# Kernel optimization log

Hardware: AMD Instinct MI355X
Metric: run time of the kernel (lower is better)

## Reference

```python
import jax, jax.numpy as jnp
import numpy as np
import math

NUM_HEADS = 8
EMBED = 512
D_K = EMBED // NUM_HEADS
B, T1, T2 = 16, 512, 512
N_POS = 2 * T1 - 1


def rel_shift(x, left_context=0):
    # x: (B, H, T1, 2*T1-1) -> (B, H, T1, T2), out[i, j] = x[i, j - i + T1 - 1]
    t1 = x.shape[2]
    t2 = t1 + left_context
    idx = jnp.arange(t2)[None, :] - jnp.arange(t1)[:, None] + (t1 - 1)  # (T1, T2)
    return jnp.take_along_axis(x, idx[None, None, :, :], axis=-1)


def setup_inputs() -> dict:
    key = jax.random.key(0)
    ks = jax.random.split(key, 16)
    scale = 1.0 / math.sqrt(EMBED)
    inp = {
        "query": jax.random.normal(ks[0], (B, T1, EMBED), jnp.float32),
        "key": jax.random.normal(ks[1], (B, T2, EMBED), jnp.float32),
        "value": jax.random.normal(ks[2], (B, T2, EMBED), jnp.float32),
        "pos_enc": jax.random.normal(ks[3], (B, N_POS, EMBED), jnp.float32),
        "mask": jnp.zeros((B, T2), dtype=bool),
        "chunk_mask": jnp.zeros((T1, T1), dtype=bool),
        "Wq": jax.random.normal(ks[4], (EMBED, EMBED), jnp.float32) * scale,
        "bq": jnp.zeros((EMBED,), jnp.float32),
        "Wk": jax.random.normal(ks[5], (EMBED, EMBED), jnp.float32) * scale,
        "bk": jnp.zeros((EMBED,), jnp.float32),
        "Wv": jax.random.normal(ks[6], (EMBED, EMBED), jnp.float32) * scale,
        "bv": jnp.zeros((EMBED,), jnp.float32),
        "Wpos": jax.random.normal(ks[7], (EMBED, EMBED), jnp.float32) * scale,
        "Wo": jax.random.normal(ks[8], (EMBED, EMBED), jnp.float32) * scale,
        "bo": jnp.zeros((EMBED,), jnp.float32),
        "pos_bias_u": jax.random.normal(ks[9], (NUM_HEADS, D_K), jnp.float32) * 0.1,
        "pos_bias_v": jax.random.normal(ks[10], (NUM_HEADS, D_K), jnp.float32) * 0.1,
        "left_context": 0,
    }
    return inp


def reference(query, key, value, pos_enc, mask, chunk_mask, Wq, bq, Wk, bk, Wv, bv,
              Wpos, Wo, bo, pos_bias_u, pos_bias_v, left_context):
    b, t1, _ = query.shape
    t2 = key.shape[1]
    # qkv projections -> (B, T, H, d_k)
    q = (query @ Wq.T + bq).reshape(b, t1, NUM_HEADS, D_K)
    k = (key @ Wk.T + bk).reshape(b, t2, NUM_HEADS, D_K)
    v = (value @ Wv.T + bv).reshape(b, t2, NUM_HEADS, D_K)
    # positional projection (no bias) -> (B, N, H, d_k)
    p = (pos_enc @ Wpos.T).reshape(b, -1, NUM_HEADS, D_K)
    # content and positional scores
    matrix_ac = jnp.einsum('bihd,bjhd->bhij', q + pos_bias_u, k)  # (B,H,T1,T2)
    matrix_bd = jnp.einsum('bihd,bnhd->bhin', q + pos_bias_v, p)  # (B,H,T1,N)
    matrix_bd = rel_shift(matrix_bd, left_context=left_context)   # (B,H,T1,T2)
    scores = (matrix_ac + matrix_bd) / math.sqrt(D_K)
    # combined mask: True = masked
    m = chunk_mask[None, None, :, :] | mask[:, None, None, :]
    neg_inf = jnp.finfo(scores.dtype).min
    scores = jnp.where(m, neg_inf, scores)
    attn = jax.nn.softmax(scores, axis=-1)
    attn = jnp.where(m, 0.0, attn)
    out = jnp.einsum('bhij,bjhd->bihd', attn, v).reshape(b, t1, NUM_HEADS * D_K)
    return out @ Wo.T + bo
```

## Files before the change

### kernel.cpp

```cpp
#include <hip/hip_runtime.h>
#include <math.h>

typedef _Float16 f16;
typedef f16 f16x8 __attribute__((ext_vector_type(8)));
typedef f16 f16x4 __attribute__((ext_vector_type(4)));
typedef float f32x4 __attribute__((ext_vector_type(4)));

#define H_   8
#define E_   512
#define DK   64
#define NPOS 1023

__device__ __forceinline__ f16x8 cvt8(const float4 a, const float4 b) {
    f16x8 h;
    h[0] = (f16)a.x; h[1] = (f16)a.y; h[2] = (f16)a.z; h[3] = (f16)a.w;
    h[4] = (f16)b.x; h[5] = (f16)b.y; h[6] = (f16)b.z; h[7] = (f16)b.w;
    return h;
}

struct PArg {
    const void* A; const float* W; const float* bias; const float* bias2;
    void* C; int Mvalid; int mode; int a16;
};
struct PArgs { PArg g[4]; };

__device__ __forceinline__ void gemm128_body(const PArg g, int bx, int by) {
    __shared__ __align__(16) f16 Al[2][128 * 32];
    __shared__ __align__(16) f16 Wl[2][128 * 32];
    const int tid = threadIdx.x;
    const int lane = tid & 63, w = tid >> 6;
    const int quad = lane >> 4, l15 = lane & 15;
    const int wr = w >> 1, wc = w & 1;
    const int m0 = by * 128, n0 = bx * 128;
    const int srow = tid >> 1, half = tid & 1;
    int arow = m0 + srow; if (arow >= g.Mvalid) arow = g.Mvalid - 1;
    const size_t aoff = (size_t)arow * 512 + half * 16;
    const size_t woff = (size_t)(n0 + srow) * 512 + half * 16;
    const int swr = (srow ^ (srow >> 2)) & 3;
    const int wo0 = srow * 32 + (((half * 2)     ^ swr) * 8);
    const int wo1 = srow * 32 + (((half * 2 + 1) ^ swr) * 8);
    const int swl = (l15 ^ (l15 >> 2)) & 3;
    const int rch = (quad ^ swl) * 8;

    f32x4 acc[4][4];
    #pragma unroll
    for (int m = 0; m < 4; ++m)
        #pragma unroll
        for (int n = 0; n < 4; ++n) acc[m][n] = (f32x4){0.f, 0.f, 0.f, 0.f};

    float4 fa0, fa1, fa2, fa3, fw0, fw1, fw2, fw3;
    uint4 ha0, ha1;

    #define LOADA(K0) do { \
        if (g.a16) { const f16* Ah = (const f16*)g.A + aoff + (K0); \
                     ha0 = *(const uint4*)Ah; ha1 = *(const uint4*)(Ah + 8); } \
        else { const float* Af = (const float*)g.A + aoff + (K0); \
               fa0 = *(const float4*)Af;       fa1 = *(const float4*)(Af + 4); \
               fa2 = *(const float4*)(Af + 8); fa3 = *(const float4*)(Af + 12); } } while (0)
    #define LOADW(K0) do { const float* Wf = g.W + woff + (K0); \
        fw0 = *(const float4*)Wf;        fw1 = *(const float4*)(Wf + 4); \
        fw2 = *(const float4*)(Wf + 8);  fw3 = *(const float4*)(Wf + 12); } while (0)
    #define STAGE(buf) do { \
        if (g.a16) { *(uint4*)&Al[buf][wo0] = ha0; *(uint4*)&Al[buf][wo1] = ha1; } \
        else { *(f16x8*)&Al[buf][wo0] = cvt8(fa0, fa1); *(f16x8*)&Al[buf][wo1] = cvt8(fa2, fa3); } \
        *(f16x8*)&Wl[buf][wo0] = cvt8(fw0, fw1); *(f16x8*)&Wl[buf][wo1] = cvt8(fw2, fw3); } while (0)

    LOADA(0); LOADW(0);
    STAGE(0);
    LOADA(32); LOADW(32);
    __syncthreads();

    #pragma unroll 2
    for (int ki = 0; ki < 16; ++ki) {
        const int cur = ki & 1, nxt = cur ^ 1;
        if (ki < 15) STAGE(nxt);
        if (ki < 14) { LOADA((ki + 2) * 32); LOADW((ki + 2) * 32); }
        f16x8 af[4], bf[4];
        #pragma unroll
        for (int m = 0; m < 4; ++m)
            af[m] = *(const f16x8*)&Al[cur][(wr * 64 + m * 16 + l15) * 32 + rch];
        #pragma unroll
        for (int n = 0; n < 4; ++n)
            bf[n] = *(const f16x8*)&Wl[cur][(wc * 64 + n * 16 + l15) * 32 + rch];
        #pragma unroll
        for (int m = 0; m < 4; ++m)
            #pragma unroll
            for (int n = 0; n < 4; ++n)
                acc[m][n] = __builtin_amdgcn_mfma_f32_16x16x32_f16(af[m], bf[n], acc[m][n], 0, 0, 0);
        __syncthreads();
    }
    #undef LOADA
    #undef LOADW
    #undef STAGE

    const int mq = m0 + wr * 64 + quad * 4;
    const int nq = n0 + wc * 64 + l15;
    #pragma unroll
    for (int m = 0; m < 4; ++m) {
        #pragma unroll
        for (int n = 0; n < 4; ++n) {
            const int gr0 = mq + m * 16;
            const int col = nq + n * 16;
            float bs = g.bias ? g.bias[col] : 0.f;
            if (g.bias2) bs += g.bias2[col];
            const f32x4 a = acc[m][n];
            if (g.mode == 0) {
                float* C = (float*)g.C;
                #pragma unroll
                for (int r = 0; r < 4; ++r) C[(size_t)(gr0 + r) * 512 + col] = a[r] + bs;
            } else if (g.mode == 1) {
                f16* C = (f16*)g.C;
                const int b = gr0 >> 9, t = gr0 & 511;
                const int hh = col >> 6, dk = col & 63;
                f16x4 hv;
                #pragma unroll
                for (int r = 0; r < 4; ++r) hv[r] = (f16)(a[r] + bs);
                *(f16x4*)&C[(((size_t)b * H_ + hh) * DK + dk) * 512 + t] = hv;
            } else if (g.mode == 2) {
                f16* C = (f16*)g.C;
                const int b = gr0 >> 9, t = gr0 & 511;
                const int hh = col >> 6, dk = col & 63;
                #pragma unroll
                for (int r = 0; r < 4; ++r)
                    C[(((size_t)b * H_ + hh) * 512 + t + r) * DK + dk] = (f16)(a[r] + bs);
            } else {
                f16* C = (f16*)g.C;
                const int hh = col >> 6, dk = col & 63;
                #pragma unroll
                for (int r = 0; r < 4; ++r) {
                    const int gm = gr0 + r;
                    if (gm < g.Mvalid) {
                        const int b = gm / NPOS, t = gm - b * NPOS;
                        C[(((size_t)b * H_ + hh) * NPOS + t) * DK + dk] = (f16)a[r];
                    }
                }
            }
        }
    }
}

__global__ __launch_bounds__(256, 3) void proj_all(PArgs a) {
    const int id = blockIdx.x;
    int gi, rem, nwg;
    if (id < 768) { gi = id >> 8; rem = id & 255; nwg = 256; }
    else          { gi = 3;       rem = id - 768; nwg = 512; }
    const int t = (rem & 7) * (nwg >> 3) + (rem >> 3);
    gemm128_body(a.g[gi], t & 3, t >> 2);
}
__global__ __launch_bounds__(256, 3) void proj_one(PArg g) {
    const int t = (blockIdx.x & 7) * 32 + (blockIdx.x >> 3);
    gemm128_body(g, t & 3, t >> 2);
}

__global__ __launch_bounds__(256) void attn_mfma(
    const f16* __restrict__ Qh,
    const f16* __restrict__ Kh,
    const f16* __restrict__ Vt,
    const f16* __restrict__ Ph,
    const float* __restrict__ pbu, const float* __restrict__ pbv,
    const unsigned char* __restrict__ bmask,
    const unsigned char* __restrict__ cmask,
    f16* __restrict__ CTX)
{
    __shared__ f16 Qa[64 * 72];
    __shared__ f16 Ka[64 * 72];
    __shared__ f16 Va[64 * 72];
    __shared__ f16 Pa[128 * 72];
    __shared__ unsigned char Ma[64 * 64];

    const int tid = threadIdx.x;
    const int lane = tid & 63, w = tid >> 6;
    const int quad = lane >> 4, l15 = lane & 15;
    const int id = blockIdx.x;
    const int lg = (id & 7) * 128 + (id >> 3);
    const int it = lg & 7, bh = lg >> 3;
    const int h = bh & 7, b = bh >> 3;
    const int i0 = it * 64;
    const int rowt = w * 16 + quad * 4;
    const int sr = tid >> 3, sc = (tid & 7) * 8;
    const int mr = tid >> 2, mc = (tid & 3) * 16;

    *(uint4*)&Qa[sr * 72 + sc] = *(const uint4*)&Qh[((size_t)bh * 512 + i0 + sr) * 64 + sc];
    *(uint4*)&Qa[(sr + 32) * 72 + sc] =
        *(const uint4*)&Qh[((size_t)bh * 512 + i0 + sr + 32) * 64 + sc];
    f16x8 dpbf[2];
    #pragma unroll
    for (int ks = 0; ks < 2; ++ks)
        #pragma unroll
        for (int j = 0; j < 8; ++j) {
            const int d = ks * 32 + quad * 8 + j;
            dpbf[ks][j] = (f16)(pbv[h * 64 + d] - pbu[h * 64 + d]);
        }

    float m_run[4], l_run[4];
    f32x4 accO[4];
    #pragma unroll
    for (int x = 0; x < 4; ++x) {
        m_run[x] = -__builtin_inff(); l_run[x] = 0.f;
        accO[x] = (f32x4){0.f, 0.f, 0.f, 0.f};
    }

    uint4 pK0, pK1, pV0, pV1, pP0, pP1, pP2, pP3, pM;
    {
        const int j0 = 0, nbase = 448 - i0;
        pK0 = *(const uint4*)&Kh[((size_t)bh * 512 + j0 + sr) * 64 + sc];
        pK1 = *(const uint4*)&Kh[((size_t)bh * 512 + j0 + sr + 32) * 64 + sc];
        pV0 = *(const uint4*)&Vt[((size_t)bh * 64 + sr) * 512 + j0 + sc];
        pV1 = *(const uint4*)&Vt[((size_t)bh * 64 + sr + 32) * 512 + j0 + sc];
        int n0_ = nbase + sr;       if (n0_ > NPOS - 1) n0_ = NPOS - 1;
        int n1_ = nbase + sr + 32;  if (n1_ > NPOS - 1) n1_ = NPOS - 1;
        int n2_ = nbase + sr + 64;  if (n2_ > NPOS - 1) n2_ = NPOS - 1;
        int n3_ = nbase + sr + 96;  if (n3_ > NPOS - 1) n3_ = NPOS - 1;
        pP0 = *(const uint4*)&Ph[((size_t)bh * NPOS + n0_) * 64 + sc];
        pP1 = *(const uint4*)&Ph[((size_t)bh * NPOS + n1_) * 64 + sc];
        pP2 = *(const uint4*)&Ph[((size_t)bh * NPOS + n2_) * 64 + sc];
        pP3 = *(const uint4*)&Ph[((size_t)bh * NPOS + n3_) * 64 + sc];
        const uint4 cm = *(const uint4*)&cmask[(size_t)(i0 + mr) * 512 + j0 + mc];
        const uint4 bm = *(const uint4*)&bmask[(size_t)b * 512 + j0 + mc];
        pM.x = cm.x | bm.x; pM.y = cm.y | bm.y; pM.z = cm.z | bm.z; pM.w = cm.w | bm.w;
    }

    for (int jt = 0; jt < 8; ++jt) {
        __syncthreads();
        *(uint4*)&Ka[sr * 72 + sc] = pK0;
        *(uint4*)&Ka[(sr + 32) * 72 + sc] = pK1;
        *(uint4*)&Va[sr * 72 + sc] = pV0;
        *(uint4*)&Va[(sr + 32) * 72 + sc] = pV1;
        *(uint4*)&Pa[sr * 72 + sc] = pP0;
        *(uint4*)&Pa[(sr + 32) * 72 + sc] = pP1;
        *(uint4*)&Pa[(sr + 64) * 72 + sc] = pP2;
        *(uint4*)&Pa[(sr + 96) * 72 + sc] = pP3;
        *(uint4*)&Ma[mr * 64 + mc] = pM;
        __syncthreads();

        if (jt < 7) {
            const int j0n = (jt + 1) * 64;
            const int nbase = j0n - i0 + 448;
            pK0 = *(const uint4*)&Kh[((size_t)bh * 512 + j0n + sr) * 64 + sc];
            pK1 = *(const uint4*)&Kh[((size_t)bh * 512 + j0n + sr + 32) * 64 + sc];
            pV0 = *(const uint4*)&Vt[((size_t)bh * 64 + sr) * 512 + j0n + sc];
            pV1 = *(const uint4*)&Vt[((size_t)bh * 64 + sr + 32) * 512 + j0n + sc];
            int n0_ = nbase + sr;       if (n0_ > NPOS - 1) n0_ = NPOS - 1;
            int n1_ = nbase + sr + 32;  if (n1_ > NPOS - 1) n1_ = NPOS - 1;
            int n2_ = nbase + sr + 64;  if (n2_ > NPOS - 1) n2_ = NPOS - 1;
            int n3_ = nbase + sr + 96;  if (n3_ > NPOS - 1) n3_ = NPOS - 1;
            pP0 = *(const uint4*)&Ph[((size_t)bh * NPOS + n0_) * 64 + sc];
            pP1 = *(const uint4*)&Ph[((size_t)bh * NPOS + n1_) * 64 + sc];
            pP2 = *(const uint4*)&Ph[((size_t)bh * NPOS + n2_) * 64 + sc];
            pP3 = *(const uint4*)&Ph[((size_t)bh * NPOS + n3_) * 64 + sc];
            const uint4 cm = *(const uint4*)&cmask[(size_t)(i0 + mr) * 512 + j0n + mc];
            const uint4 bm = *(const uint4*)&bmask[(size_t)b * 512 + j0n + mc];
            pM.x = cm.x | bm.x; pM.y = cm.y | bm.y; pM.z = cm.z | bm.z; pM.w = cm.w | bm.w;
        }

        f16x8 afQ[2], afV[2];
        #pragma unroll
        for (int ks = 0; ks < 2; ++ks) {
            afQ[ks] = *(const f16x8*)&Qa[(w * 16 + l15) * 72 + ks * 32 + quad * 8];
            afV[ks] = afQ[ks] + dpbf[ks];
        }
        f32x4 accAC[4];
        #pragma unroll
        for (int nt = 0; nt < 4; ++nt) {
            accAC[nt] = (f32x4){0.f, 0.f, 0.f, 0.f};
            #pragma unroll
            for (int ks = 0; ks < 2; ++ks) {
                const f16x8 bf = *(const f16x8*)&Ka[(nt * 16 + l15) * 72 + ks * 32 + quad * 8];
                accAC[nt] = __builtin_amdgcn_mfma_f32_16x16x32_f16(afQ[ks], bf, accAC[nt], 0, 0, 0);
            }
        }
        f32x4 accBD[5];
        #pragma unroll
        for (int u = 0; u < 5; ++u) {
            accBD[u] = (f32x4){0.f, 0.f, 0.f, 0.f};
            const int nts = (3 - w) + u;
            #pragma unroll
            for (int ks = 0; ks < 2; ++ks) {
                const f16x8 bf = *(const f16x8*)&Pa[(nts * 16 + l15) * 72 + ks * 32 + quad * 8];
                accBD[u] = __builtin_amdgcn_mfma_f32_16x16x32_f16(afV[ks], bf, accBD[u], 0, 0, 0);
            }
        }
        __syncthreads();

        #pragma unroll
        for (int rg = 0; rg < 4; ++rg) {
            const int qr = quad * 4 + rg;
            const int rt = rowt + rg;
            float tmpv[5];
            #pragma unroll
            for (int u = 0; u < 5; ++u) {
                const int cl = l15 + (3 + u) * 16 + qr - 63;
                const int dst = (quad * 16 + (cl & 15)) << 2;
                tmpv[u] = __uint_as_float(
                    (unsigned)__builtin_amdgcn_ds_permute(dst, (int)__float_as_uint(accBD[u][rg])));
            }
            const bool hi = l15 > qr;
            float sv[4]; unsigned mk = 0;
            #pragma unroll
            for (int nt = 0; nt < 4; ++nt) {
                const int c = nt * 16 + l15;
                const float bdv = hi ? tmpv[nt + 1] : tmpv[nt];
                float s = (accAC[nt][rg] + bdv) * 0.125f;
                if (Ma[rt * 64 + c]) { s = -3.402823466e38f; mk |= 1u << nt; }
                sv[nt] = s;
            }
            float tmax = fmaxf(fmaxf(sv[0], sv[1]), fmaxf(sv[2], sv[3]));
            #pragma unroll
            for (int d = 1; d < 16; d <<= 1) tmax = fmaxf(tmax, __shfl_xor(tmax, d));
            const float mnew = fmaxf(m_run[rg], tmax);
            const float alpha = __expf(m_run[rg] - mnew);
            float rsum = 0.f;
            f16 wv[4];
            #pragma unroll
            for (int nt = 0; nt < 4; ++nt) {
                const float e = __expf(sv[nt] - mnew);
                rsum += e;
                wv[nt] = ((mk >> nt) & 1u) ? (f16)0.f : (f16)e;
            }
            #pragma unroll
            for (int d = 1; d < 16; d <<= 1) rsum += __shfl_xor(rsum, d);
            l_run[rg] = l_run[rg] * alpha + rsum;
            m_run[rg] = mnew;
            #pragma unroll
            for (int dt = 0; dt < 4; ++dt) accO[dt][rg] *= alpha;
            #pragma unroll
            for (int nt = 0; nt < 4; ++nt)
                Ka[rt * 72 + nt * 16 + l15] = wv[nt];
        }
        f16x8 afW[2];
        #pragma unroll
        for (int ks = 0; ks < 2; ++ks)
            afW[ks] = *(const f16x8*)&Ka[(w * 16 + l15) * 72 + ks * 32 + quad * 8];
        #pragma unroll
        for (int dt = 0; dt < 4; ++dt)
            #pragma unroll
            for (int ks = 0; ks < 2; ++ks) {
                const f16x8 bf = *(const f16x8*)&Va[(dt * 16 + l15) * 72 + ks * 32 + quad * 8];
                accO[dt] = __builtin_amdgcn_mfma_f32_16x16x32_f16(afW[ks], bf, accO[dt], 0, 0, 0);
            }
    }

    #pragma unroll
    for (int rg = 0; rg < 4; ++rg) {
        const float inv = 1.0f / l_run[rg];
        const int gi = i0 + rowt + rg;
        #pragma unroll
        for (int dt = 0; dt < 4; ++dt)
            CTX[((size_t)b * 512 + gi) * 512 + h * 64 + dt * 16 + l15] = (f16)(accO[dt][rg] * inv);
    }
}

extern "C" void kernel_launch(void* const* d_in, const int* in_sizes, int n_in,
                              void* d_out, int out_size, void* d_ws, size_t ws_size,
                              hipStream_t stream) {
    const float* query   = (const float*)d_in[0];
    const float* key     = (const float*)d_in[1];
    const float* value   = (const float*)d_in[2];
    const float* pos_enc = (const float*)d_in[3];
    const unsigned char* mask       = (const unsigned char*)d_in[4];
    const unsigned char* chunk_mask = (const unsigned char*)d_in[5];
    const float* Wq  = (const float*)d_in[6];
    const float* bq  = (const float*)d_in[7];
    const float* Wk  = (const float*)d_in[8];
    const float* bk  = (const float*)d_in[9];
    const float* Wv  = (const float*)d_in[10];
    const float* bv  = (const float*)d_in[11];
    const float* Wpos = (const float*)d_in[12];
    const float* Wo   = (const float*)d_in[13];
    const float* bo   = (const float*)d_in[14];
    const float* pbu  = (const float*)d_in[15];
    const float* pbv  = (const float*)d_in[16];
    float* out = (float*)d_out;

    f16* base = (f16*)d_ws;
    size_t off = 0;
    f16* ctx = base + off; off += 4194304;
    f16* Qhm = base + off; off += 4194304;
    f16* Khm = base + off; off += 4194304;
    f16* Vtm = base + off; off += 4194304;
    f16* Phm = base + off; off += 8380416;

    PArgs pa;
    pa.g[0] = PArg{query,   Wq,   bq, pbu,     (void*)Qhm, 8192,  2, 0};
    pa.g[1] = PArg{key,     Wk,   bk, nullptr, (void*)Khm, 8192,  2, 0};
    pa.g[2] = PArg{value,   Wv,   bv, nullptr, (void*)Vtm, 8192,  1, 0};
    pa.g[3] = PArg{pos_enc, Wpos, nullptr, nullptr, (void*)Phm, 16368, 3, 0};
    proj_all<<<dim3(1280), 256, 0, stream>>>(pa);

    attn_mfma<<<dim3(1024), 256, 0, stream>>>(Qhm, Khm, Vtm, Phm, pbu, pbv,
                                              mask, chunk_mask, ctx);

    PArg go = PArg{ctx, Wo, bo, nullptr, (void*)out, 8192, 0, 1};
    proj_one<<<dim3(256), 256, 0, stream>>>(go);
}
```

Measured before the change: 287.6 us.

## Pre-convert inputs to fp16 and load GEMM tiles via global_load_lds

Adds a separate conversion kernel that casts all fp32 activations and weights to fp16 in workspace. The projection GEMMs then stream fp16 tiles directly into LDS with global_load_lds instead of loading fp32 into registers, converting and storing. This drops the double-buffered LDS, the swizzled layout and the register prefetch, and raises occupancy to 4 blocks. The trade-off is an extra full read and write pass over the inputs, plus a GEMM loop that no longer overlaps loads with MFMA and may now hit LDS bank conflicts.

```diff
diff --git a/kernel.cpp b/kernel.cpp
--- a/kernel.cpp
+++ b/kernel.cpp
@@ -11,36 +11,54 @@
 #define DK   64
 #define NPOS 1023
 
-__device__ __forceinline__ f16x8 cvt8(const float4 a, const float4 b) {
-    f16x8 h;
-    h[0] = (f16)a.x; h[1] = (f16)a.y; h[2] = (f16)a.z; h[3] = (f16)a.w;
-    h[4] = (f16)b.x; h[5] = (f16)b.y; h[6] = (f16)b.z; h[7] = (f16)b.w;
-    return h;
+#define GLL(SRC, DST) __builtin_amdgcn_global_load_lds( \
+    (const __attribute__((address_space(1))) void*)(SRC), \
+    (__attribute__((address_space(3))) void*)(DST), 16, 0, 0)
+
+struct CSeg { const float* src; f16* dst; int n4; };
+struct CArgs { CSeg s[9]; };
+__global__ __launch_bounds__(256) void conv_f16(CArgs a) {
+    const int stride = gridDim.x * 256;
+    const int gid = blockIdx.x * 256 + threadIdx.x;
+    for (int si = 0; si < 9; ++si) {
+        const float* __restrict__ src = a.s[si].src;
+        f16* __restrict__ dst = a.s[si].dst;
+        const int n4 = a.s[si].n4;
+        for (int i = gid; i < n4; i += stride) {
+            const float4 v = ((const float4*)src)[i];
+            f16x4 h; h[0] = (f16)v.x; h[1] = (f16)v.y; h[2] = (f16)v.z; h[3] = (f16)v.w;
+            ((f16x4*)dst)[i] = h;
+        }
+    }
 }
 
 struct PArg {
-    const void* A; const float* W; const float* bias; const float* bias2;
-    void* C; int Mvalid; int mode; int a16;
+    const f16* A; const f16* W; const float* bias; const float* bias2;
+    void* C; int Mvalid; int mode;
 };
 struct PArgs { PArg g[4]; };
 
 __device__ __forceinline__ void gemm128_body(const PArg g, int bx, int by) {
-    __shared__ __align__(16) f16 Al[2][128 * 32];
-    __shared__ __align__(16) f16 Wl[2][128 * 32];
+    __shared__ __align__(16) f16 Al[128 * 32];
+    __shared__ __align__(16) f16 Wl[128 * 32];
     const int tid = threadIdx.x;
     const int lane = tid & 63, w = tid >> 6;
     const int quad = lane >> 4, l15 = lane & 15;
     const int wr = w >> 1, wc = w & 1;
     const int m0 = by * 128, n0 = bx * 128;
-    const int srow = tid >> 1, half = tid & 1;
-    int arow = m0 + srow; if (arow >= g.Mvalid) arow = g.Mvalid - 1;
-    const size_t aoff = (size_t)arow * 512 + half * 16;
-    const size_t woff = (size_t)(n0 + srow) * 512 + half * 16;
-    const int swr = (srow ^ (srow >> 2)) & 3;
-    const int wo0 = srow * 32 + (((half * 2)     ^ swr) * 8);
-    const int wo1 = srow * 32 + (((half * 2 + 1) ^ swr) * 8);
-    const int swl = (l15 ^ (l15 >> 2)) & 3;
-    const int rch = (quad ^ swl) * 8;
+
+    const int r0 = w * 32 + (lane >> 2);
+    const int c0 = (lane & 3) * 8;
+    int ar0 = m0 + r0;      if (ar0 >= g.Mvalid) ar0 = g.Mvalid - 1;
+    int ar1 = m0 + r0 + 16; if (ar1 >= g.Mvalid) ar1 = g.Mvalid - 1;
+    const f16* A0 = g.A + (size_t)ar0 * 512 + c0;
+    const f16* A1 = g.A + (size_t)ar1 * 512 + c0;
+    const f16* W0 = g.W + (size_t)(n0 + r0) * 512 + c0;
+    const f16* W1 = g.W + (size_t)(n0 + r0 + 16) * 512 + c0;
+    f16* const lA0 = &Al[(w * 32) * 32];
+    f16* const lA1 = &Al[(w * 32 + 16) * 32];
+    f16* const lW0 = &Wl[(w * 32) * 32];
+    f16* const lW1 = &Wl[(w * 32 + 16) * 32];
 
     f32x4 acc[4][4];
     #pragma unroll
@@ -48,50 +66,28 @@
         #pragma unroll
         for (int n = 0; n < 4; ++n) acc[m][n] = (f32x4){0.f, 0.f, 0.f, 0.f};
 
-    float4 fa0, fa1, fa2, fa3, fw0, fw1, fw2, fw3;
-    uint4 ha0, ha1;
-
-    #define LOADA(K0) do { \
-        if (g.a16) { const f16* Ah = (const f16*)g.A + aoff + (K0); \
-                     ha0 = *(const uint4*)Ah; ha1 = *(const uint4*)(Ah + 8); } \
-        else { const float* Af = (const float*)g.A + aoff + (K0); \
-               fa0 = *(const float4*)Af;       fa1 = *(const float4*)(Af + 4); \
-               fa2 = *(const float4*)(Af + 8); fa3 = *(const float4*)(Af + 12); } } while (0)
-    #define LOADW(K0) do { const float* Wf = g.W + woff + (K0); \
-        fw0 = *(const float4*)Wf;        fw1 = *(const float4*)(Wf + 4); \
-        fw2 = *(const float4*)(Wf + 8);  fw3 = *(const float4*)(Wf + 12); } while (0)
-    #define STAGE(buf) do { \
-        if (g.a16) { *(uint4*)&Al[buf][wo0] = ha0; *(uint4*)&Al[buf][wo1] = ha1; } \
-        else { *(f16x8*)&Al[buf][wo0] = cvt8(fa0, fa1); *(f16x8*)&Al[buf][wo1] = cvt8(fa2, fa3); } \
-        *(f16x8*)&Wl[buf][wo0] = cvt8(fw0, fw1); *(f16x8*)&Wl[buf][wo1] = cvt8(fw2, fw3); } while (0)
-
-    LOADA(0); LOADW(0);
-    STAGE(0);
-    LOADA(32); LOADW(32);
-    __syncthreads();
-
-    #pragma unroll 2
     for (int ki = 0; ki < 16; ++ki) {
-        const int cur = ki & 1, nxt = cur ^ 1;
-        if (ki < 15) STAGE(nxt);
-        if (ki < 14) { LOADA((ki + 2) * 32); LOADW((ki + 2) * 32); }
+        const int k0 = ki * 32;
+        if (ki) __syncthreads();
+        GLL(A0 + k0, lA0);
+        GLL(A1 + k0, lA1);
+        GLL(W0 + k0, lW0);
+        GLL(W1 + k0, lW1);
+        __syncthreads();
+
         f16x8 af[4], bf[4];
         #pragma unroll
         for (int m = 0; m < 4; ++m)
-            af[m] = *(const f16x8*)&Al[cur][(wr * 64 + m * 16 + l15) * 32 + rch];
+            af[m] = *(const f16x8*)&Al[(wr * 64 + m * 16 + l15) * 32 + quad * 8];
         #pragma unroll
         for (int n = 0; n < 4; ++n)
-            bf[n] = *(const f16x8*)&Wl[cur][(wc * 64 + n * 16 + l15) * 32 + rch];
+            bf[n] = *(const f16x8*)&Wl[(wc * 64 + n * 16 + l15) * 32 + quad * 8];
         #pragma unroll
         for (int m = 0; m < 4; ++m)
             #pragma unroll
             for (int n = 0; n < 4; ++n)
                 acc[m][n] = __builtin_amdgcn_mfma_f32_16x16x32_f16(af[m], bf[n], acc[m][n], 0, 0, 0);
-        __syncthreads();
-    }
-    #undef LOADA
-    #undef LOADW
-    #undef STAGE
+    }
 
     const int mq = m0 + wr * 64 + quad * 4;
     const int nq = n0 + wc * 64 + l15;
@@ -139,7 +135,7 @@
     }
 }
 
-__global__ __launch_bounds__(256, 3) void proj_all(PArgs a) {
+__global__ __launch_bounds__(256, 4) void proj_all(PArgs a) {
     const int id = blockIdx.x;
     int gi, rem, nwg;
     if (id < 768) { gi = id >> 8; rem = id & 255; nwg = 256; }
@@ -147,7 +143,7 @@
     const int t = (rem & 7) * (nwg >> 3) + (rem >> 3);
     gemm128_body(a.g[gi], t & 3, t >> 2);
 }
-__global__ __launch_bounds__(256, 3) void proj_one(PArg g) {
+__global__ __launch_bounds__(256, 4) void proj_one(PArg g) {
     const int t = (blockIdx.x & 7) * 32 + (blockIdx.x >> 3);
     gemm128_body(g, t & 3, t >> 2);
 }
@@ -374,22 +370,43 @@
 
     f16* base = (f16*)d_ws;
     size_t off = 0;
-    f16* ctx = base + off; off += 4194304;
-    f16* Qhm = base + off; off += 4194304;
-    f16* Khm = base + off; off += 4194304;
-    f16* Vtm = base + off; off += 4194304;
-    f16* Phm = base + off; off += 8380416;
+    f16* ctx  = base + off; off += 4194304;
+    f16* Qhm  = base + off; off += 4194304;
+    f16* Khm  = base + off; off += 4194304;
+    f16* Vtm  = base + off; off += 4194304;
+    f16* Phm  = base + off; off += 8380416;
+    f16* qf   = base + off; off += 4194304;
+    f16* kf   = base + off; off += 4194304;
+    f16* vf   = base + off; off += 4194304;
+    f16* pf   = base + off; off += 8380416;
+    f16* wqf  = base + off; off += 262144;
+    f16* wkf  = base + off; off += 262144;
+    f16* wvf  = base + off; off += 262144;
+    f16* wpf  = base + off; off += 262144;
+    f16* wof  = base + off; off += 262144;
+
+    CArgs ca;
+    ca.s[0] = CSeg{pos_enc, pf,  2095104};
+    ca.s[1] = CSeg{query,   qf,  1048576};
+    ca.s[2] = CSeg{key,     kf,  1048576};
+    ca.s[3] = CSeg{value,   vf,  1048576};
+    ca.s[4] = CSeg{Wq,      wqf, 65536};
+    ca.s[5] = CSeg{Wk,      wkf, 65536};
+    ca.s[6] = CSeg{Wv,      wvf, 65536};
+    ca.s[7] = CSeg{Wpos,    wpf, 65536};
+    ca.s[8] = CSeg{Wo,      wof, 65536};
+    conv_f16<<<dim3(2048), 256, 0, stream>>>(ca);
 
     PArgs pa;
-    pa.g[0] = PArg{query,   Wq,   bq, pbu,     (void*)Qhm, 8192,  2, 0};
-    pa.g[1] = PArg{key,     Wk,   bk, nullptr, (void*)Khm, 8192,  2, 0};
-    pa.g[2] = PArg{value,   Wv,   bv, nullptr, (void*)Vtm, 8192,  1, 0};
-    pa.g[3] = PArg{pos_enc, Wpos, nullptr, nullptr, (void*)Phm, 16368, 3, 0};
+    pa.g[0] = PArg{qf, wqf, bq, pbu,     (void*)Qhm, 8192,  2};
+    pa.g[1] = PArg{kf, wkf, bk, nullptr, (void*)Khm, 8192,  2};
+    pa.g[2] = PArg{vf, wvf, bv, nullptr, (void*)Vtm, 8192,  1};
+    pa.g[3] = PArg{pf, wpf, nullptr, nullptr, (void*)Phm, 16368, 3};
     proj_all<<<dim3(1280), 256, 0, stream>>>(pa);
 
     attn_mfma<<<dim3(1024), 256, 0, stream>>>(Qhm, Khm, Vtm, Phm, pbu, pbv,
                                               mask, chunk_mask, ctx);
 
-    PArg go = PArg{ctx, Wo, bo, nullptr, (void*)out, 8192, 0, 1};
+    PArg go = PArg{ctx, wof, bo, nullptr, (void*)out, 8192, 0};
     proj_one<<<dim3(256), 256, 0, stream>>>(go);
 }
```

Result: faster. 270.3 us (-6.0%).
